# Optimization experiments

Measured on AMD Instinct MI355X. Metric: run time of the kernel, lower is better.

The kernel has to match this reference:

```python
import jax, jax.numpy as jnp
import numpy as np

# geometry constants from init_kwargs
VX, VY, VZ = 0.1, 0.1, 4.0
X_OFF, Y_OFF, Z_OFF = VX / 2 - 51.2, VY / 2 - 51.2, VZ / 2 - 3.0
GY, GX = 1024, 1024  # round((51.2-(-51.2))/0.1)
NUM_BEV = 8
BN_EPS = 1e-3


def setup_inputs() -> dict:
    key = jax.random.key(0)
    k1, k2, k3, k4, k5, k6 = jax.random.split(key, 6)
    N, P, C_in, C_out = 40000, 32, 10, 64
    voxel_features = jax.random.normal(k1, (N, P, 4), jnp.float32)
    voxel_num_points = jax.random.randint(k2, (N,), 1, P + 1, jnp.int32)
    bb = jax.random.randint(k3, (N,), 0, 2, jnp.int32)
    yy = jax.random.randint(k4, (N,), 0, GY, jnp.int32)
    xx = jax.random.randint(k5, (N,), 0, GX, jnp.int32)
    coords = jnp.stack([bb, jnp.zeros((N,), jnp.int32), yy, xx], axis=1)
    record_len = jnp.array([N // 2, N - N // 2], jnp.int32)
    W = jax.random.normal(k6, (C_in, C_out), jnp.float32) * 0.1
    gamma = jnp.ones((C_out,), jnp.float32)
    beta = jnp.zeros((C_out,), jnp.float32)
    run_mean = jnp.zeros((C_out,), jnp.float32)
    run_var = jnp.ones((C_out,), jnp.float32)
    return {"voxel_features": voxel_features, "W": W, "gamma": gamma,
            "beta": beta, "run_mean": run_mean, "run_var": run_var,
            "voxel_num_points": voxel_num_points, "coords": coords,
            "record_len": record_len}


def reference(voxel_features, W, gamma, beta, run_mean, run_var,
              voxel_num_points, coords, record_len):
    N, P, _ = voxel_features.shape
    npts = voxel_num_points.astype(voxel_features.dtype)  # [N]
    xyz = voxel_features[:, :, :3]

    # cluster offset feature
    points_mean = xyz.sum(axis=1, keepdims=True) / npts[:, None, None]
    f_cluster = xyz - points_mean

    # pillar-center offset feature
    cx = coords[:, 3].astype(voxel_features.dtype)[:, None] * VX + X_OFF
    cy = coords[:, 2].astype(voxel_features.dtype)[:, None] * VY + Y_OFF
    cz = coords[:, 1].astype(voxel_features.dtype)[:, None] * VZ + Z_OFF
    f_center = jnp.stack([xyz[:, :, 0] - cx, xyz[:, :, 1] - cy,
                          xyz[:, :, 2] - cz], axis=-1)

    features = jnp.concatenate([voxel_features, f_cluster, f_center], axis=-1)  # [N,P,10]

    # padding mask
    mask = (voxel_num_points[:, None] > jnp.arange(P, dtype=jnp.int32)[None, :])
    mask = mask[..., None].astype(voxel_features.dtype)  # [N,P,1]
    features = features * mask

    # PFN layer: Linear(10->64, no bias) + BN(eval) + ReLU + max over points
    x = jnp.einsum('npc,cd->npd', features, W)  # [N,P,64]
    x = (x - run_mean) * jax.lax.rsqrt(run_var + BN_EPS) * gamma + beta
    x = jax.nn.relu(x)
    pillar_features = x.max(axis=1)  # [N,64]

    # hand-crafted BEV stats
    safe_n = jnp.clip(npts, 1.0)[:, None]  # [N,1]
    num_points_norm = npts[:, None] / P
    intensity = voxel_features[:, :, 3:4]
    mean_intensity = (intensity * mask).sum(axis=1) / safe_n
    z = xyz[:, :, 2:3]
    mean_height = (z * mask).sum(axis=1) / safe_n
    max_height = (z * mask + (1 - mask) * -1e6).max(axis=1)
    min_height = (z * mask + (1 - mask) * 1e6).min(axis=1)
    height_span = max_height - min_height
    pm = (xyz * mask).sum(axis=1, keepdims=True) / safe_n[:, :, None]
    var_xyz = (((xyz - pm) ** 2) * mask).sum(axis=1) / safe_n  # [N,3]
    pillar_bev = jnp.concatenate([num_points_norm, mean_intensity, mean_height,
                                  max_height, height_span, var_xyz[:, 0:1],
                                  var_xyz[:, 1:2], var_xyz[:, 2:3]], axis=1)  # [N,8]

    batch_size = record_len.shape[0]
    b = jnp.clip(coords[:, 0], 0, batch_size - 1)
    y_idx = coords[:, 2]
    x_idx = coords[:, 3]
    vox_bev = jnp.zeros((batch_size, NUM_BEV, GY, GX), voxel_features.dtype)
    vox_bev = vox_bev.at[b, :, y_idx, x_idx].set(pillar_bev)

    return pillar_features, vox_bev
```

## Files before the change

kernel.cpp:

```cpp
#include <hip/hip_runtime.h>

#define GYD 1024
#define GXD 1024
#define NUM_BEV 8

__device__ __forceinline__ float rdlanef(float x, int l) {
    return __int_as_float(__builtin_amdgcn_readlane(__float_as_int(x), l));
}
template <int CTRL, int ROWMASK>
__device__ __forceinline__ float dppf(float x, float oldv) {
    return __int_as_float(__builtin_amdgcn_update_dpp(
        __float_as_int(oldv), __float_as_int(x), CTRL, ROWMASK, 0xF, false));
}
__device__ __forceinline__ float dsum32(float x) {
    x += dppf<0x111, 0xF>(x, 0.f);
    x += dppf<0x112, 0xF>(x, 0.f);
    x += dppf<0x114, 0xF>(x, 0.f);
    x += dppf<0x118, 0xF>(x, 0.f);
    x += dppf<0x142, 0xA>(x, 0.f);
    return x;
}
__device__ __forceinline__ float dmax32(float x) {
    x = fmaxf(x, dppf<0x111, 0xF>(x, x));
    x = fmaxf(x, dppf<0x112, 0xF>(x, x));
    x = fmaxf(x, dppf<0x114, 0xF>(x, x));
    x = fmaxf(x, dppf<0x118, 0xF>(x, x));
    x = fmaxf(x, dppf<0x142, 0xA>(x, x));
    return x;
}
__device__ __forceinline__ float dmin32(float x) {
    x = fminf(x, dppf<0x111, 0xF>(x, x));
    x = fminf(x, dppf<0x112, 0xF>(x, x));
    x = fminf(x, dppf<0x114, 0xF>(x, x));
    x = fminf(x, dppf<0x118, 0xF>(x, x));
    x = fminf(x, dppf<0x142, 0xA>(x, x));
    return x;
}

__device__ __forceinline__ float2 f2(float a)             { return make_float2(a, a); }
__device__ __forceinline__ float2 add2(float2 a, float2 b){ return make_float2(a.x+b.x, a.y+b.y); }
__device__ __forceinline__ float2 mul2(float2 a, float2 b){ return make_float2(a.x*b.x, a.y*b.y); }
__device__ __forceinline__ float2 fma2(float2 a, float2 b, float2 c){
    return make_float2(fmaf(a.x,b.x,c.x), fmaf(a.y,b.y,c.y));
}
__device__ __forceinline__ float2 max2(float2 a, float2 b){
    return make_float2(fmaxf(a.x,b.x), fmaxf(a.y,b.y));
}

__global__ __launch_bounds__(256) void pillar_kernel(
    const float4* __restrict__ vf,
    const float* __restrict__ W,
    const float* __restrict__ gammap, const float* __restrict__ betap,
    const float* __restrict__ rmeanp, const float* __restrict__ rvarp,
    const int* __restrict__ npts_arr,
    const int* __restrict__ coords,
    float* __restrict__ pillar_out,
    float* __restrict__ bev_vals,
    int* __restrict__ winner,
    int N, int bs)
{
    __shared__ float4 pts[4][2][32];
    const int wid  = threadIdx.x >> 6;
    const int lane = threadIdx.x & 63;
    const int half = lane >> 5;
    const int sl   = lane & 31;
    const int n0   = blockIdx.x * 8 + wid * 2;
    const int n    = n0 + half;
    const bool valid = (n < N);
    const int nn = valid ? n : 0;

    const int c0 = sl, c1 = sl + 32;
    float2 w_[10];
#pragma unroll
    for (int k = 0; k < 10; ++k)
        w_[k] = make_float2(W[k * 64 + c0], W[k * 64 + c1]);
    const float2 gg = make_float2(gammap[c0], gammap[c1]);
    const float2 bb = make_float2(betap[c0],  betap[c1]);
    const float2 rmn= make_float2(rmeanp[c0], rmeanp[c1]);
    const float2 rvr= make_float2(rvarp[c0],  rvarp[c1]);

    const int npts = npts_arr[nn];
    const int4 crd = ((const int4*)coords)[nn];
    const float cx = (float)crd.w * 0.1f - 51.15f;
    const float cy = (float)crd.z * 0.1f - 51.15f;
    const float cz = (float)crd.y * 4.0f - 1.0f;

    float4 v = make_float4(0.f, 0.f, 0.f, 0.f);
    if (valid) v = vf[(size_t)nn * 32 + sl];
    const bool pv = sl < npts;
    const float m = pv ? 1.f : 0.f;

    pts[wid][half][sl] = v;
    const float4 p0 = pts[wid][half][0];
    if (!pv) pts[wid][half][sl] = p0;

    const float sx   = dsum32(v.x);
    const float sy   = dsum32(v.y);
    const float sz   = dsum32(v.z);
    const float smx  = dsum32(v.x * m);
    const float smy  = dsum32(v.y * m);
    const float smz  = dsum32(v.z * m);
    const float smI  = dsum32(v.w * m);
    const float sx2  = dsum32(v.x * v.x * m);
    const float sy2  = dsum32(v.y * v.y * m);
    const float sz2  = dsum32(v.z * v.z * m);
    const float maxz = dmax32(pv ? v.z : -1e6f);
    const float minz = dmin32(pv ? v.z :  1e6f);

    const float invn = 1.f / (float)npts;
    const float mx = (half ? rdlanef(sx, 63) : rdlanef(sx, 31)) * invn;
    const float my = (half ? rdlanef(sy, 63) : rdlanef(sy, 31)) * invn;
    const float mz = (half ? rdlanef(sz, 63) : rdlanef(sz, 31)) * invn;

    const int nA = __builtin_amdgcn_readlane(npts, 0);
    const int nB = __builtin_amdgcn_readlane(npts, 32);
    const int nmax = nA > nB ? nA : nB;

    const float2 scale = mul2(gg, make_float2(rsqrtf(rvr.x + 1e-3f), rsqrtf(rvr.y + 1e-3f)));
    const float2 shift = fma2(f2(-1.f), mul2(rmn, scale), bb);
    const float2 A = mul2(add2(add2(w_[0], w_[4]), w_[7]), scale);
    const float2 B = mul2(add2(add2(w_[1], w_[5]), w_[8]), scale);
    const float2 C = mul2(add2(add2(w_[2], w_[6]), w_[9]), scale);
    const float2 D = mul2(w_[3], scale);
    float2 E = mul2(f2(mx), w_[4]);
    E = fma2(f2(my), w_[5], E);
    E = fma2(f2(mz), w_[6], E);
    E = fma2(f2(cx), w_[7], E);
    E = fma2(f2(cy), w_[8], E);
    E = fma2(f2(cz), w_[9], E);
    const float2 bse = fma2(f2(-1.f), mul2(E, scale), shift);

    float2 acc = make_float2(-1e30f, -1e30f);
#pragma unroll 2
    for (int p = 0; p < nmax; ++p) {
        const float4 q = pts[wid][half][p];
        const float2 t = fma2(f2(q.x), A, fma2(f2(q.y), B,
                         fma2(f2(q.z), C, fma2(f2(q.w), D, bse))));
        acc = max2(acc, t);
    }
    if (npts < 32) acc = max2(acc, shift);
    acc = max2(acc, f2(0.f));

    if (valid) {
        pillar_out[(size_t)n * 64 + c0] = acc.x;
        pillar_out[(size_t)n * 64 + c1] = acc.y;
    }

    if (valid && sl == 31) {
        const float fn = (float)npts;
        const float pmx = smx * invn, pmy = smy * invn, pmz = smz * invn;
        const float vvx = fmaf(-pmx, pmx, sx2 * invn);
        const float vvy = fmaf(-pmy, pmy, sy2 * invn);
        const float vvz = fmaf(-pmz, pmz, sz2 * invn);
        float4* bvp = (float4*)&bev_vals[(size_t)n * 8];
        bvp[0] = make_float4(fn * (1.f / 32.f), smI * invn, pmz, maxz);
        bvp[1] = make_float4(maxz - minz, vvx, vvy, vvz);
        const int b = crd.x < 0 ? 0 : (crd.x > bs - 1 ? bs - 1 : crd.x);
        atomicMax(&winner[(b * GYD + crd.z) * GXD + crd.w], n + 1);
    }
}

__global__ __launch_bounds__(256) void bev_fill(
    const int4* __restrict__ winner4,
    const float* __restrict__ bev_vals,
    float* __restrict__ vox_bev, int bs, int N)
{
    const int gidx = blockIdx.x * 256 + threadIdx.x;
    const int4 w = winner4[gidx];
    const bool k0 = (w.x > 0) & (w.x <= N);
    const bool k1 = (w.y > 0) & (w.y <= N);
    const bool k2 = (w.z > 0) & (w.z <= N);
    const bool k3 = (w.w > 0) & (w.w <= N);
    const int c0 = gidx << 2;
    const int b  = c0 >> 20;
    const int yx = c0 & ((1 << 20) - 1);
    float* basep = vox_bev + (((size_t)b * NUM_BEV) << 20) + yx;
    if (!(k0 | k1 | k2 | k3)) {
        const float4 z4 = make_float4(0.f, 0.f, 0.f, 0.f);
#pragma unroll
        for (int k = 0; k < NUM_BEV; ++k)
            *(float4*)(basep + ((size_t)k << 20)) = z4;
    } else {
#pragma unroll
        for (int k = 0; k < NUM_BEV; ++k) {
            float4 o;
            o.x = k0 ? bev_vals[(size_t)(w.x - 1) * 8 + k] : 0.f;
            o.y = k1 ? bev_vals[(size_t)(w.y - 1) * 8 + k] : 0.f;
            o.z = k2 ? bev_vals[(size_t)(w.z - 1) * 8 + k] : 0.f;
            o.w = k3 ? bev_vals[(size_t)(w.w - 1) * 8 + k] : 0.f;
            *(float4*)(basep + ((size_t)k << 20)) = o;
        }
    }
}

extern "C" void kernel_launch(void* const* d_in, const int* in_sizes, int n_in,
                              void* d_out, int out_size, void* d_ws, size_t ws_size,
                              hipStream_t stream) {
    const float4* vf    = (const float4*)d_in[0];
    const float* W      = (const float*)d_in[1];
    const float* gammap = (const float*)d_in[2];
    const float* betap  = (const float*)d_in[3];
    const float* rmeanp = (const float*)d_in[4];
    const float* rvarp  = (const float*)d_in[5];
    const int* npts     = (const int*)d_in[6];
    const int* coords   = (const int*)d_in[7];
    const int N  = in_sizes[6];
    const int bs = in_sizes[8];

    float* pillar_out = (float*)d_out;
    float* vox_bev    = (float*)d_out + (size_t)N * 64;

    int* winner     = (int*)d_ws;
    float* bev_vals = (float*)((char*)d_ws + (size_t)bs * GYD * GXD * sizeof(int));


    const int blocksA = (N + 7) / 8;
    pillar_kernel<<<blocksA, 256, 0, stream>>>(vf, W, gammap, betap, rmeanp, rvarp,
                                               npts, coords, pillar_out, bev_vals,
                                               winner, N, bs);
    const int blocksB = (bs << 20) / (256 * 4);
    bev_fill<<<blocksB, 256, 0, stream>>>((const int4*)winner, bev_vals, vox_bev, bs, N);
}
```

Measured before the change: 129.0 us.

## Make pillar kernel persistent with software-prefetched next pillar pair

Launches a fixed grid of 1280 blocks in place of one block per 8 pillars. Each wave loops over pillar pairs with a grid stride and prefetches the next pair's points, npts and coords while computing the current one. This amortizes the per-wave loads of W and the BN parameters (now float2 loads) and hides global load latency. It also switches to float2 stores for the pillar output. The cost is fewer waves in flight and extra registers for the prefetched data. The pillar kernel is likely a small part of the total, since bev_fill writes 64MB.

Measured after the change: 139.8 us. 1.08x slower.

```diff
diff --git a/kernel.cpp b/kernel.cpp
--- a/kernel.cpp
+++ b/kernel.cpp
@@ -3,6 +3,9 @@
 #define GYD 1024
 #define GXD 1024
 #define NUM_BEV 8
+#define PBLK 1280
+#define PTHR 256
+#define PWAVES (PBLK * PTHR / 64)
 
 __device__ __forceinline__ float rdlanef(float x, int l) {
     return __int_as_float(__builtin_amdgcn_readlane(__float_as_int(x), l));
@@ -36,7 +39,6 @@
     x = fminf(x, dppf<0x142, 0xA>(x, x));
     return x;
 }
-
 __device__ __forceinline__ float2 f2(float a)             { return make_float2(a, a); }
 __device__ __forceinline__ float2 add2(float2 a, float2 b){ return make_float2(a.x+b.x, a.y+b.y); }
 __device__ __forceinline__ float2 mul2(float2 a, float2 b){ return make_float2(a.x*b.x, a.y*b.y); }
@@ -64,99 +66,128 @@
     const int lane = threadIdx.x & 63;
     const int half = lane >> 5;
     const int sl   = lane & 31;
-    const int n0   = blockIdx.x * 8 + wid * 2;
-    const int n    = n0 + half;
-    const bool valid = (n < N);
-    const int nn = valid ? n : 0;
-
-    const int c0 = sl, c1 = sl + 32;
+    const int gwave = (blockIdx.x * PTHR + threadIdx.x) >> 6;
+    const int npairs = (N + 1) >> 1;
+
+    const float2* W2 = (const float2*)W;
     float2 w_[10];
 #pragma unroll
-    for (int k = 0; k < 10; ++k)
-        w_[k] = make_float2(W[k * 64 + c0], W[k * 64 + c1]);
-    const float2 gg = make_float2(gammap[c0], gammap[c1]);
-    const float2 bb = make_float2(betap[c0],  betap[c1]);
-    const float2 rmn= make_float2(rmeanp[c0], rmeanp[c1]);
-    const float2 rvr= make_float2(rvarp[c0],  rvarp[c1]);
-
-    const int npts = npts_arr[nn];
-    const int4 crd = ((const int4*)coords)[nn];
-    const float cx = (float)crd.w * 0.1f - 51.15f;
-    const float cy = (float)crd.z * 0.1f - 51.15f;
-    const float cz = (float)crd.y * 4.0f - 1.0f;
-
-    float4 v = make_float4(0.f, 0.f, 0.f, 0.f);
-    if (valid) v = vf[(size_t)nn * 32 + sl];
-    const bool pv = sl < npts;
-    const float m = pv ? 1.f : 0.f;
-
-    pts[wid][half][sl] = v;
-    const float4 p0 = pts[wid][half][0];
-    if (!pv) pts[wid][half][sl] = p0;
-
-    const float sx   = dsum32(v.x);
-    const float sy   = dsum32(v.y);
-    const float sz   = dsum32(v.z);
-    const float smx  = dsum32(v.x * m);
-    const float smy  = dsum32(v.y * m);
-    const float smz  = dsum32(v.z * m);
-    const float smI  = dsum32(v.w * m);
-    const float sx2  = dsum32(v.x * v.x * m);
-    const float sy2  = dsum32(v.y * v.y * m);
-    const float sz2  = dsum32(v.z * v.z * m);
-    const float maxz = dmax32(pv ? v.z : -1e6f);
-    const float minz = dmin32(pv ? v.z :  1e6f);
-
-    const float invn = 1.f / (float)npts;
-    const float mx = (half ? rdlanef(sx, 63) : rdlanef(sx, 31)) * invn;
-    const float my = (half ? rdlanef(sy, 63) : rdlanef(sy, 31)) * invn;
-    const float mz = (half ? rdlanef(sz, 63) : rdlanef(sz, 31)) * invn;
-
-    const int nA = __builtin_amdgcn_readlane(npts, 0);
-    const int nB = __builtin_amdgcn_readlane(npts, 32);
-    const int nmax = nA > nB ? nA : nB;
-
+    for (int k = 0; k < 10; ++k) w_[k] = W2[k * 32 + sl];
+    const float2 gg  = ((const float2*)gammap)[sl];
+    const float2 bb  = ((const float2*)betap)[sl];
+    const float2 rmn = ((const float2*)rmeanp)[sl];
+    const float2 rvr = ((const float2*)rvarp)[sl];
     const float2 scale = mul2(gg, make_float2(rsqrtf(rvr.x + 1e-3f), rsqrtf(rvr.y + 1e-3f)));
     const float2 shift = fma2(f2(-1.f), mul2(rmn, scale), bb);
     const float2 A = mul2(add2(add2(w_[0], w_[4]), w_[7]), scale);
     const float2 B = mul2(add2(add2(w_[1], w_[5]), w_[8]), scale);
     const float2 C = mul2(add2(add2(w_[2], w_[6]), w_[9]), scale);
     const float2 D = mul2(w_[3], scale);
-    float2 E = mul2(f2(mx), w_[4]);
-    E = fma2(f2(my), w_[5], E);
-    E = fma2(f2(mz), w_[6], E);
-    E = fma2(f2(cx), w_[7], E);
-    E = fma2(f2(cy), w_[8], E);
-    E = fma2(f2(cz), w_[9], E);
-    const float2 bse = fma2(f2(-1.f), mul2(E, scale), shift);
-
-    float2 acc = make_float2(-1e30f, -1e30f);
+
+    int pr = gwave;
+    bool has = pr < npairs;
+    int n_cur = pr * 2 + half;
+    bool val_cur = has && (n_cur < N);
+    int nn = val_cur ? n_cur : 0;
+    float4 v_cur = make_float4(0.f, 0.f, 0.f, 0.f);
+    int np_cur = 1;
+    int4 crd_cur = make_int4(0, 0, 0, 0);
+    if (has) {
+        v_cur   = val_cur ? vf[(size_t)nn * 32 + sl] : v_cur;
+        np_cur  = npts_arr[nn];
+        crd_cur = ((const int4*)coords)[nn];
+    }
+
+    while (has) {
+        const int pr_nxt = pr + PWAVES;
+        const bool has_nxt = pr_nxt < npairs;
+        const int n_nxt = pr_nxt * 2 + half;
+        const bool val_nxt = has_nxt && (n_nxt < N);
+        const int mm = val_nxt ? n_nxt : 0;
+        float4 v_nxt = make_float4(0.f, 0.f, 0.f, 0.f);
+        int np_nxt = 1;
+        int4 crd_nxt = make_int4(0, 0, 0, 0);
+        if (has_nxt) {
+            v_nxt   = val_nxt ? vf[(size_t)mm * 32 + sl] : v_nxt;
+            np_nxt  = npts_arr[mm];
+            crd_nxt = ((const int4*)coords)[mm];
+        }
+
+        const float4 v = v_cur;
+        const int npts = np_cur;
+        const int4 crd = crd_cur;
+        const int n = n_cur;
+        const bool valid = val_cur;
+        const float cx = (float)crd.w * 0.1f - 51.15f;
+        const float cy = (float)crd.z * 0.1f - 51.15f;
+        const float cz = (float)crd.y * 4.0f - 1.0f;
+        const bool pv = sl < npts;
+        const float m = pv ? 1.f : 0.f;
+
+        pts[wid][half][sl] = v;
+        const float4 p0 = pts[wid][half][0];
+        if (!pv) pts[wid][half][sl] = p0;
+
+        const float sx   = dsum32(v.x);
+        const float sy   = dsum32(v.y);
+        const float sz   = dsum32(v.z);
+        const float smx  = dsum32(v.x * m);
+        const float smy  = dsum32(v.y * m);
+        const float smz  = dsum32(v.z * m);
+        const float smI  = dsum32(v.w * m);
+        const float sx2  = dsum32(v.x * v.x * m);
+        const float sy2  = dsum32(v.y * v.y * m);
+        const float sz2  = dsum32(v.z * v.z * m);
+        const float maxz = dmax32(pv ? v.z : -1e6f);
+        const float minz = dmin32(pv ? v.z :  1e6f);
+
+        const float invn = 1.f / (float)npts;
+        const float mx = (half ? rdlanef(sx, 63) : rdlanef(sx, 31)) * invn;
+        const float my = (half ? rdlanef(sy, 63) : rdlanef(sy, 31)) * invn;
+        const float mz = (half ? rdlanef(sz, 63) : rdlanef(sz, 31)) * invn;
+
+        float2 E = mul2(f2(mx), w_[4]);
+        E = fma2(f2(my), w_[5], E);
+        E = fma2(f2(mz), w_[6], E);
+        E = fma2(f2(cx), w_[7], E);
+        E = fma2(f2(cy), w_[8], E);
+        E = fma2(f2(cz), w_[9], E);
+        const float2 bse = fma2(f2(-1.f), mul2(E, scale), shift);
+
+        const int cA = __builtin_amdgcn_readlane(npts, 0);
+        const int cB = __builtin_amdgcn_readlane(npts, 32);
+        const int nmax = cA > cB ? cA : cB;
+
+        float2 acc = f2(-1e30f);
 #pragma unroll 2
-    for (int p = 0; p < nmax; ++p) {
-        const float4 q = pts[wid][half][p];
-        const float2 t = fma2(f2(q.x), A, fma2(f2(q.y), B,
-                         fma2(f2(q.z), C, fma2(f2(q.w), D, bse))));
-        acc = max2(acc, t);
-    }
-    if (npts < 32) acc = max2(acc, shift);
-    acc = max2(acc, f2(0.f));
-
-    if (valid) {
-        pillar_out[(size_t)n * 64 + c0] = acc.x;
-        pillar_out[(size_t)n * 64 + c1] = acc.y;
-    }
-
-    if (valid && sl == 31) {
-        const float fn = (float)npts;
-        const float pmx = smx * invn, pmy = smy * invn, pmz = smz * invn;
-        const float vvx = fmaf(-pmx, pmx, sx2 * invn);
-        const float vvy = fmaf(-pmy, pmy, sy2 * invn);
-        const float vvz = fmaf(-pmz, pmz, sz2 * invn);
-        float4* bvp = (float4*)&bev_vals[(size_t)n * 8];
-        bvp[0] = make_float4(fn * (1.f / 32.f), smI * invn, pmz, maxz);
-        bvp[1] = make_float4(maxz - minz, vvx, vvy, vvz);
-        const int b = crd.x < 0 ? 0 : (crd.x > bs - 1 ? bs - 1 : crd.x);
-        atomicMax(&winner[(b * GYD + crd.z) * GXD + crd.w], n + 1);
+        for (int p = 0; p < nmax; ++p) {
+            const float4 q = pts[wid][half][p];
+            const float2 t = fma2(f2(q.x), A, fma2(f2(q.y), B,
+                             fma2(f2(q.z), C, fma2(f2(q.w), D, bse))));
+            acc = max2(acc, t);
+        }
+        if (npts < 32) acc = max2(acc, shift);
+        acc = max2(acc, f2(0.f));
+
+        if (valid)
+            ((float2*)(pillar_out + (size_t)n * 64))[sl] = acc;
+
+        if (valid && sl == 31) {
+            const float fn = (float)npts;
+            const float pmx = smx * invn, pmy = smy * invn, pmz = smz * invn;
+            const float vvx = fmaf(-pmx, pmx, sx2 * invn);
+            const float vvy = fmaf(-pmy, pmy, sy2 * invn);
+            const float vvz = fmaf(-pmz, pmz, sz2 * invn);
+            float4* bvp = (float4*)&bev_vals[(size_t)n * 8];
+            bvp[0] = make_float4(fn * (1.f / 32.f), smI * invn, pmz, maxz);
+            bvp[1] = make_float4(maxz - minz, vvx, vvy, vvz);
+            const int b = crd.x < 0 ? 0 : (crd.x > bs - 1 ? bs - 1 : crd.x);
+            atomicMax(&winner[(b * GYD + crd.z) * GXD + crd.w], n + 1);
+        }
+
+        pr = pr_nxt; has = has_nxt;
+        n_cur = n_nxt; val_cur = val_nxt;
+        v_cur = v_nxt; np_cur = np_nxt; crd_cur = crd_nxt;
     }
 }
 
@@ -214,10 +245,9 @@
     float* bev_vals = (float*)((char*)d_ws + (size_t)bs * GYD * GXD * sizeof(int));
 
 
-    const int blocksA = (N + 7) / 8;
-    pillar_kernel<<<blocksA, 256, 0, stream>>>(vf, W, gammap, betap, rmeanp, rvarp,
-                                               npts, coords, pillar_out, bev_vals,
-                                               winner, N, bs);
+    pillar_kernel<<<PBLK, PTHR, 0, stream>>>(vf, W, gammap, betap, rmeanp, rvarp,
+                                             npts, coords, pillar_out, bev_vals,
+                                             winner, N, bs);
     const int blocksB = (bs << 20) / (256 * 4);
     bev_fill<<<blocksB, 256, 0, stream>>>((const int4*)winner, bev_vals, vox_bev, bs, N);
 }
```
